# Kernel tuning notes

Hardware: AMD Instinct MI355X
Metric: run time of the kernel (lower is better)

Reference implementation:

```python
import jax, jax.numpy as jnp
import numpy as np
import math

H = 1024
NH = 16
D = H // NH  # 64
EPS = 1e-5


def _layernorm(x, g, b):
    mu = jnp.mean(x, axis=-1, keepdims=True)
    var = jnp.mean(jnp.square(x - mu), axis=-1, keepdims=True)
    return (x - mu) * jax.lax.rsqrt(var + EPS) * g + b


def setup_inputs() -> dict:
    key = jax.random.key(0)
    ks = jax.random.split(key, 12)
    B, T = 2, 2048
    q = jax.random.normal(ks[0], (B, T, H), jnp.float32)
    k = jax.random.normal(ks[1], (B, T, H), jnp.float32)
    v = jax.random.normal(ks[2], (B, T, H), jnp.float32)
    pad_mask = jax.random.randint(ks[3], (B, T), 0, 2) > 0
    s = 0.02
    Wq = jax.random.normal(ks[4], (H, H), jnp.float32) * s
    Wk = jax.random.normal(ks[5], (H, H), jnp.float32) * s
    Wv = jax.random.normal(ks[6], (H, H), jnp.float32) * s
    Wo = jax.random.normal(ks[7], (H, H), jnp.float32) * s
    W1 = jax.random.normal(ks[8], (4 * H, H), jnp.float32) * s
    b1 = jnp.zeros((4 * H,), jnp.float32)
    W2 = jax.random.normal(ks[9], (H, 4 * H), jnp.float32) * s
    b2 = jnp.zeros((H,), jnp.float32)
    g1 = jnp.ones((H,), jnp.float32); be1 = jnp.zeros((H,), jnp.float32)
    g2 = jnp.ones((H,), jnp.float32); be2 = jnp.zeros((H,), jnp.float32)
    return dict(q=q, k=k, v=v, pad_mask=pad_mask, Wq=Wq, Wk=Wk, Wv=Wv, Wo=Wo,
                W1=W1, b1=b1, W2=W2, b2=b2, g1=g1, be1=be1, g2=g2, be2=be2)


def reference(q, k, v, pad_mask, Wq, Wk, Wv, Wo, W1, b1, W2, b2, g1, be1, g2, be2):
    B, Tq, _ = q.shape
    Tv = v.shape[1]
    # torch nn.Linear: x @ W.T
    Q = (q @ Wq.T).reshape(B, NH, Tq, D)  # faithful to torch .view head split
    K = (k @ Wk.T).reshape(B, NH, Tv, D)
    V = (v @ Wv.T).reshape(B, NH, Tv, D)
    logits = jnp.einsum('baih,bajh->baij', Q, K)  # [B,NH,Tq,Tv]
    neg_inf = jnp.float32(-jnp.inf)
    logits = jnp.where(pad_mask[:, None, None, :], logits, neg_inf)
    attn = jax.nn.softmax(logits / math.sqrt(D), axis=-1)
    # post-softmax query-mask multiply (custom)
    attn = attn * pad_mask[:, None, :, None].astype(attn.dtype)
    h = jnp.einsum('baij,bajh->baih', attn, V).reshape(B, Tq, H)
    h = h @ Wo.T
    h = _layernorm(q + h, g1, be1)
    ff = jax.nn.gelu(h @ W1.T + b1, approximate=False) @ W2.T + b2  # dropout = identity (eval)
    return _layernorm(h + ff, g2, be2)
```

## Files before the change

kernel.cpp:

```cpp
#include <hip/hip_runtime.h>

typedef unsigned short u16;
typedef unsigned int u32;
typedef __attribute__((ext_vector_type(8))) __bf16 bf16x8;
typedef __attribute__((ext_vector_type(4))) float f32x4;
typedef __attribute__((ext_vector_type(16))) float f32x16;
typedef __attribute__((ext_vector_type(4))) unsigned short u16x4;
typedef __attribute__((ext_vector_type(8))) unsigned short u16x8;

#define LOG2E 1.44269504088896340736f

__device__ __forceinline__ u16 f2bf(float f) {
  union { float f; unsigned u; } c; c.f = f;
  unsigned r = c.u + 0x7FFFu + ((c.u >> 16) & 1u);
  return (u16)(r >> 16);
}
__device__ __forceinline__ float bf2f(u16 h) {
  union { unsigned u; float f; } c; c.u = ((unsigned)h) << 16;
  return c.f;
}

__device__ __forceinline__ void gload_lds16(const u16* g, u16* l) {
  __builtin_amdgcn_global_load_lds((const __attribute__((address_space(1))) unsigned int*)g,
                                   (__attribute__((address_space(3))) unsigned int*)l, 16, 0, 0);
}

__device__ __forceinline__ float gelu_fast(float x) {
  float z = fabsf(x) * 0.70710678118654752f;
  float t = 1.0f / (1.0f + 0.3275911f * z);
  float poly = t * (0.254829592f + t * (-0.284496736f + t * (1.421413741f +
               t * (-1.453152027f + t * 1.061405429f))));
  float e = __builtin_amdgcn_exp2f(-z * z * LOG2E);
  float erfz = 1.0f - poly * e;
  float s = (x >= 0.0f) ? erfz : -erfz;
  return 0.5f * x * (1.0f + s);
}

__global__ __launch_bounds__(256) void cvt_all(
    const float* __restrict__ s0, const float* __restrict__ s1, const float* __restrict__ s2,
    const float* __restrict__ s3, const float* __restrict__ s4, const float* __restrict__ s5,
    const float* __restrict__ s6, const float* __restrict__ s7, const float* __restrict__ s8,
    u16* __restrict__ d0, u16* __restrict__ d1, u16* __restrict__ d2,
    u16* __restrict__ d3, u16* __restrict__ d4, u16* __restrict__ d5,
    u16* __restrict__ d6, u16* __restrict__ d7, u16* __restrict__ d8) {
  int i = blockIdx.x * 256 + threadIdx.x;
  if (i >= 6291456) return;
  const float* src; u16* dst; int off;
  if (i < 3145728) {
    if (i < 1048576)      { src = s0; dst = d0; off = 0; }
    else if (i < 2097152) { src = s1; dst = d1; off = 1048576; }
    else                  { src = s2; dst = d2; off = 2097152; }
  } else if (i < 4194304) {
    if (i < 3407872)      { src = s3; dst = d3; off = 3145728; }
    else if (i < 3670016) { src = s4; dst = d4; off = 3407872; }
    else if (i < 3932160) { src = s5; dst = d5; off = 3670016; }
    else                  { src = s6; dst = d6; off = 3932160; }
  } else {
    if (i < 5242880)      { src = s7; dst = d7; off = 4194304; }
    else                  { src = s8; dst = d8; off = 5242880; }
  }
  int j = i - off;
  f32x4 v = ((const f32x4*)src)[j];
  u16x4 o;
  o[0] = f2bf(v[0]); o[1] = f2bf(v[1]); o[2] = f2bf(v[2]); o[3] = f2bf(v[3]);
  ((u16x4*)dst)[j] = o;
}

__global__ void build_masks(const void* __restrict__ pm, float* __restrict__ maskbias,
                            float* __restrict__ qmask, int n) {
  __shared__ int sflag;
  if (threadIdx.x == 0) sflag = 0;
  __syncthreads();
  const unsigned* pw = (const unsigned*)pm;
  int nwords = n / 4;
  int local = 0;
  for (int i = threadIdx.x; i < nwords; i += blockDim.x)
    if (pw[i] > 1u) local = 1;
  if (local) atomicOr(&sflag, 1);
  __syncthreads();
  bool isbool = (sflag != 0);
  for (int i = threadIdx.x; i < n; i += blockDim.x) {
    int m = isbool ? (int)((const unsigned char*)pm)[i] : ((const int*)pm)[i];
    maskbias[i] = m ? 0.0f : -2e30f;
    qmask[i]    = m ? 1.0f : 0.0f;
  }
}

template<int EPI>
__device__ __forceinline__ void gemm_core(const u16* __restrict__ A, const u16* __restrict__ Bw,
                                          const float* __restrict__ bias, u16* __restrict__ C,
                                          int N, int Kstride, int Klen, int bn, int bm, int tid) {
  __shared__ u16 smem[3][8192];
  int wave = tid >> 6, lane = tid & 63;
  int l15 = lane & 15, l4 = lane >> 4;
  int wr = (wave >> 1) * 32;
  int wc = (wave & 1) * 64;
  int mrow0 = bm * 128, ncol0 = bn * 128;
  int srow = lane >> 2;
  int scol = (lane & 3) * 8;

  const u16* asrc = A  + (size_t)(mrow0 + wave * 16 + srow) * Kstride + scol;
  const u16* bsrc = Bw + (size_t)(ncol0 + wave * 16 + srow) * Kstride + scol;
  u16* ad = &smem[0][wave * 512];
  u16* bd = &smem[0][4096 + wave * 512];

  auto stage = [&](int buf, int k0) {
    gload_lds16(asrc + k0, ad + buf * 8192);
    gload_lds16(bsrc + k0, bd + buf * 8192);
  };

  f32x4 acc[2][4];
#pragma unroll
  for (int i = 0; i < 2; i++)
#pragma unroll
    for (int j = 0; j < 4; j++) acc[i][j] = (f32x4)0.0f;

  int nsteps = Klen >> 5;
  stage(0, 0);
  stage(1, 32);
  int cur = 0;
  for (int s = 0; s < nsteps; s++) {
    if (s + 1 < nsteps) {
      asm volatile("s_waitcnt vmcnt(2)" ::: "memory");
    } else {
      asm volatile("s_waitcnt vmcnt(0)" ::: "memory");
    }
    __builtin_amdgcn_s_barrier();
    if (s + 2 < nsteps) {
      int nb = cur + 2; if (nb >= 3) nb -= 3;
      stage(nb, (s + 2) << 5);
    }
    const u16* as = &smem[cur][0];
    const u16* bs = &smem[cur][4096];
    bf16x8 af[2], bfr[4];
#pragma unroll
    for (int mi = 0; mi < 2; mi++) af[mi]  = *(const bf16x8*)(as + (wr + mi * 16 + l15) * 32 + l4 * 8);
#pragma unroll
    for (int ni = 0; ni < 4; ni++) bfr[ni] = *(const bf16x8*)(bs + (wc + ni * 16 + l15) * 32 + l4 * 8);
#pragma unroll
    for (int mi = 0; mi < 2; mi++)
#pragma unroll
      for (int ni = 0; ni < 4; ni++)
        acc[mi][ni] = __builtin_amdgcn_mfma_f32_16x16x32_bf16(af[mi], bfr[ni], acc[mi][ni], 0, 0, 0);
    cur++; if (cur >= 3) cur = 0;
  }

  __syncthreads();
  u16* ct = &smem[0][0];
#pragma unroll
  for (int ni = 0; ni < 4; ni++) {
    int gcol = ncol0 + wc + ni * 16 + l15;
    float bv = (EPI > 0) ? bias[gcol] : 0.0f;
#pragma unroll
    for (int mi = 0; mi < 2; mi++) {
#pragma unroll
      for (int r = 0; r < 4; r++) {
        float v = acc[mi][ni][r] + bv;
        if (EPI == 2) v = gelu_fast(v);
        ct[(wr + mi * 16 + l4 * 4 + r) * 136 + wc + ni * 16 + l15] = f2bf(v);
      }
    }
  }
  __syncthreads();
  int lrow = tid >> 2, cq = tid & 3;
#pragma unroll
  for (int j = 0; j < 4; j++) {
    int col = cq * 8 + j * 32;
    u16x8 vv = *(const u16x8*)(ct + lrow * 136 + col);
    *(u16x8*)(C + (size_t)(mrow0 + lrow) * N + ncol0 + col) = vv;
  }
}

template<int EPI>
__global__ __launch_bounds__(512, 4) void gemm_bt(const u16* __restrict__ A, const u16* __restrict__ Bw,
                                                  const float* __restrict__ bias, u16* __restrict__ C,
                                                  int N, int K) {
  gemm_core<EPI>(A, Bw, bias, C, N, K, K, blockIdx.x, blockIdx.y, threadIdx.x);
}

__global__ __launch_bounds__(512, 4) void gemm_splitk(const u16* __restrict__ A, const u16* __restrict__ Bw,
                                                      u16* __restrict__ P, int N, int Kstride, int Kc) {
  int z = blockIdx.z;
  size_t M = (size_t)gridDim.y * 128;
  gemm_core<0>(A + (size_t)z * Kc, Bw + (size_t)z * Kc, nullptr,
               P + (size_t)z * M * N, N, Kstride, Kc, blockIdx.x, blockIdx.y, threadIdx.x);
}

__global__ __launch_bounds__(512, 4) void gemm_qkv(const u16* __restrict__ qb, const u16* __restrict__ kb,
                                                   const u16* __restrict__ vb,
                                                   const u16* __restrict__ wq, const u16* __restrict__ wk,
                                                   const u16* __restrict__ wv,
                                                   u16* __restrict__ Qo, u16* __restrict__ Ko, u16* __restrict__ Vo) {
  const u16* A; const u16* W; u16* C;
  if (blockIdx.z == 0)      { A = qb; W = wq; C = Qo; }
  else if (blockIdx.z == 1) { A = kb; W = wk; C = Ko; }
  else                      { A = vb; W = wv; C = Vo; }
  gemm_core<0>(A, W, nullptr, C, 1024, 1024, 1024, blockIdx.x, blockIdx.y, threadIdx.x);
}

__global__ __launch_bounds__(256) void transpose64(const u16* __restrict__ in, u16* __restrict__ out) {
  int bh = blockIdx.y, tb = blockIdx.x;
  __shared__ u16 tile[64 * 72];
  int tid = threadIdx.x;
#pragma unroll
  for (int it = 0; it < 2; it++) {
    int idx = it * 256 + tid;
    int r = idx >> 3, c8 = (idx & 7) * 8;
    u16x8 v = *(const u16x8*)(in + ((size_t)bh * 2048 + tb * 64 + r) * 64 + c8);
    int byte = ((r * 72 + c8) * 2) ^ (((r >> 3) & 7) << 4);
    *(u16x8*)((char*)tile + byte) = v;
  }
  __syncthreads();
#pragma unroll
  for (int it = 0; it < 2; it++) {
    int idx = it * 256 + tid;
    int d = idx >> 3, t8 = (idx & 7) * 8;
    u16x8 o;
#pragma unroll
    for (int e = 0; e < 8; e++) {
      int t = t8 + e;
      int byte = ((t * 72 + d) * 2) ^ (((t >> 3) & 7) << 4);
      o[e] = *(const u16*)((const char*)tile + byte);
    }
    *(u16x8*)(out + ((size_t)bh * 64 + d) * 2048 + tb * 64 + t8) = o;
  }
}

__global__ __launch_bounds__(256, 4) void attn4(const u16* __restrict__ Q, const u16* __restrict__ Kg,
                                                const u16* __restrict__ VT,
                                                const float* __restrict__ maskbias,
                                                u16* __restrict__ O0, u16* __restrict__ O1,
                                                float* __restrict__ Ms, float* __restrict__ Ss) {
  const int T = 2048;
  int bh = blockIdx.x;
  int qt = blockIdx.y;
  int sp = blockIdx.z;
  int b = bh >> 4;
  const u16* Qh = Q  + (size_t)bh * T * 64;
  const u16* Kh = Kg + (size_t)bh * T * 64;
  const u16* Vh = VT + (size_t)bh * T * 64;
  u16* Oh = (sp ? O1 : O0) + (size_t)bh * T * 64;
  const float* mb = maskbias + b * T + sp * 1024;
  int tid = threadIdx.x, w = tid >> 6, l = tid & 63;
  int q32 = l & 31, h = l >> 5;
  int qbase = qt * 128 + w * 32;
  const float C = 0.125f * LOG2E;

  __shared__ u16 Ks[2][4096];
  __shared__ u16 Vs[2][4096];

  bf16x8 qf[4];
#pragma unroll
  for (int dc = 0; dc < 4; dc++)
    qf[dc] = *(const bf16x8*)(Qh + (size_t)(qbase + q32) * 64 + dc * 16 + h * 8);

  int rl = l >> 3, ob = (l & 7) * 16;
  int osw = ob ^ (rl << 4);
  int r0 = w * 16 + rl, r1 = w * 16 + 8 + rl;
  const u16* pK0 = Kh + (size_t)(sp * 1024 + r0) * 64 + (osw >> 1);
  const u16* pK1 = Kh + (size_t)(sp * 1024 + r1) * 64 + (osw >> 1);
  const u16* pV0 = Vh + (size_t)r0 * 2048 + sp * 1024 + (osw >> 1);
  const u16* pV1 = Vh + (size_t)r1 * 2048 + sp * 1024 + (osw >> 1);
  u16* dK0 = &Ks[0][0] + (w * 16) * 64;
  u16* dK1 = &Ks[0][0] + (w * 16 + 8) * 64;
  u16* dV0 = &Vs[0][0] + (w * 16) * 64;
  u16* dV1 = &Vs[0][0] + (w * 16 + 8) * 64;

  auto stage = [&](int buf) {
    gload_lds16(pK0, dK0 + buf * 4096);
    gload_lds16(pK1, dK1 + buf * 4096);
    gload_lds16(pV0, dV0 + buf * 4096);
    gload_lds16(pV1, dV1 + buf * 4096);
    pK0 += 4096; pK1 += 4096; pV0 += 64; pV1 += 64;
  };

  f32x16 acc[2];
  acc[0] = (f32x16)0.0f; acc[1] = (f32x16)0.0f;
  float m_ = -3e30f, s_ = 0.0f;

  int swz = (q32 & 7) << 4;

  stage(0);
  for (int t = 0; t < 16; t++) {
    int cur = t & 1;
    __syncthreads();
    if (t < 15) stage(cur ^ 1);
    const char* ksb = (const char*)(&Ks[0][0] + cur * 4096);
    const char* vsb = (const char*)(&Vs[0][0] + cur * 4096);

    bf16x8 kf[2][4];
#pragma unroll
    for (int kvc = 0; kvc < 2; kvc++)
#pragma unroll
      for (int dc = 0; dc < 4; dc++)
        kf[kvc][dc] = *(const bf16x8*)(ksb + (kvc * 32 + q32) * 128 + ((dc * 32 + h * 16) ^ swz));

    f32x16 st[2];
    st[0] = (f32x16)0.0f; st[1] = (f32x16)0.0f;
#pragma unroll
    for (int kvc = 0; kvc < 2; kvc++)
#pragma unroll
      for (int dc = 0; dc < 4; dc++)
        st[kvc] = __builtin_amdgcn_mfma_f32_32x32x16_bf16(kf[kvc][dc], qf[dc], st[kvc], 0, 0, 0);

    float p[32];
    float pmax = -3e30f;
#pragma unroll
    for (int kvc = 0; kvc < 2; kvc++) {
#pragma unroll
      for (int g = 0; g < 4; g++) {
        f32x4 mv = *(const f32x4*)(mb + t * 64 + kvc * 32 + g * 8 + h * 4);
#pragma unroll
        for (int r = 0; r < 4; r++) {
          float val = st[kvc][g * 4 + r] * C + mv[r];
          p[kvc * 16 + g * 4 + r] = val;
          pmax = fmaxf(pmax, val);
        }
      }
    }
    pmax = fmaxf(pmax, __shfl_xor(pmax, 32));

    if (__any(pmax - m_ > 8.0f)) {
      float mnew = fmaxf(m_, pmax);
      float fsc = __builtin_amdgcn_exp2f(m_ - mnew);
      s_ *= fsc;
      m_ = mnew;
#pragma unroll
      for (int g = 0; g < 4; g++)
#pragma unroll
        for (int r = 0; r < 4; r++) {
          float f = __shfl(fsc, g * 8 + h * 4 + r);
          acc[0][g * 4 + r] *= f;
          acc[1][g * 4 + r] *= f;
        }
    }

    float rsum = 0.0f;
    u32 wds[16];
#pragma unroll
    for (int i = 0; i < 16; i++) {
      float a = __builtin_amdgcn_exp2f(p[2 * i] - m_);
      float bq = __builtin_amdgcn_exp2f(p[2 * i + 1] - m_);
      rsum += a + bq;
      union { __bf16 h2[2]; u32 u; } cv;
      cv.h2[0] = (__bf16)a; cv.h2[1] = (__bf16)bq;
      wds[i] = cv.u;
    }
    rsum += __shfl_xor(rsum, 32);
    s_ += rsum;

#pragma unroll
    for (int kvc = 0; kvc < 2; kvc++) {
      int bse = kvc * 8;
      u32 sw0 = __shfl_xor(wds[bse + 0], 32), sw1 = __shfl_xor(wds[bse + 1], 32);
      u32 sw2 = __shfl_xor(wds[bse + 2], 32), sw3 = __shfl_xor(wds[bse + 3], 32);
      u32 sw4 = __shfl_xor(wds[bse + 4], 32), sw5 = __shfl_xor(wds[bse + 5], 32);
      u32 sw6 = __shfl_xor(wds[bse + 6], 32), sw7 = __shfl_xor(wds[bse + 7], 32);
      union { u32 u[4]; bf16x8 v; } pa0, pa1;
      pa0.u[0] = h ? sw2 : wds[bse + 0];
      pa0.u[1] = h ? sw3 : wds[bse + 1];
      pa0.u[2] = h ? wds[bse + 2] : sw0;
      pa0.u[3] = h ? wds[bse + 3] : sw1;
      pa1.u[0] = h ? sw6 : wds[bse + 4];
      pa1.u[1] = h ? sw7 : wds[bse + 5];
      pa1.u[2] = h ? wds[bse + 6] : sw4;
      pa1.u[3] = h ? wds[bse + 7] : sw5;
#pragma unroll
      for (int cl = 0; cl < 2; cl++) {
        bf16x8 pa = cl ? pa1.v : pa0.v;
        int cg = kvc * 2 + cl;
#pragma unroll
        for (int dblk = 0; dblk < 2; dblk++) {
          bf16x8 vf = *(const bf16x8*)(vsb + (dblk * 32 + q32) * 128 + ((cg * 32 + h * 16) ^ swz));
          acc[dblk] = __builtin_amdgcn_mfma_f32_32x32x16_bf16(pa, vf, acc[dblk], 0, 0, 0);
        }
      }
    }
  }

#pragma unroll
  for (int g = 0; g < 4; g++) {
#pragma unroll
    for (int r = 0; r < 4; r++) {
      int row = g * 8 + h * 4 + r;
#pragma unroll
      for (int dblk = 0; dblk < 2; dblk++)
        Oh[(size_t)(qbase + row) * 64 + dblk * 32 + q32] = f2bf(acc[dblk][g * 4 + r]);
    }
  }
  if (h == 0) {
    int ro = sp * 65536 + bh * 2048 + qbase + q32;
    Ms[ro] = m_;
    Ss[ro] = s_;
  }
}

__global__ __launch_bounds__(256) void attn_combine(const u16* __restrict__ O0, const u16* __restrict__ O1,
                                                    const float* __restrict__ Ms, const float* __restrict__ Ss,
                                                    const float* __restrict__ qmaskf, u16* __restrict__ out) {
  int idx = blockIdx.x * 256 + threadIdx.x;
  int row = idx >> 3;
  int d8 = (idx & 7) * 8;
  int bh = row >> 11, r = row & 2047, b = bh >> 4;
  float m0 = Ms[row], m1 = Ms[65536 + row];
  float mstar = fmaxf(m0, m1);
  float w0 = __builtin_amdgcn_exp2f(m0 - mstar);
  float w1 = __builtin_amdgcn_exp2f(m1 - mstar);
  float den = w0 * Ss[row] + w1 * Ss[65536 + row];
  float scale = qmaskf[b * 2048 + r] / den;
  size_t base = (size_t)row * 64 + d8;
  u16x8 a0 = *(const u16x8*)(O0 + base);
  u16x8 a1 = *(const u16x8*)(O1 + base);
  u16x8 o;
#pragma unroll
  for (int e = 0; e < 8; e++)
    o[e] = f2bf((w0 * bf2f(a0[e]) + w1 * bf2f(a1[e])) * scale);
  *(u16x8*)(out + base) = o;
}

template<int NP, int A_F32, int ADD_BIAS, int OUT_F32>
__global__ __launch_bounds__(256) void add_ln_multi(const void* __restrict__ Ap,
                                                    const u16* __restrict__ P0, const u16* __restrict__ P1,
                                                    const u16* __restrict__ P2, const u16* __restrict__ P3,
                                                    const float* __restrict__ bias,
                                                    const float* __restrict__ g, const float* __restrict__ be,
                                                    void* __restrict__ outp) {
  int row = blockIdx.x, tid = threadIdx.x;
  int lane = tid & 63, wave = tid >> 6;
  size_t rb = (size_t)row * 1024;
  float x[4];
  if (A_F32) {
    f32x4 a = ((const f32x4*)((const float*)Ap + rb))[tid];
#pragma unroll
    for (int j = 0; j < 4; j++) x[j] = a[j];
  } else {
    u16x4 au = ((const u16x4*)((const u16*)Ap + rb))[tid];
#pragma unroll
    for (int j = 0; j < 4; j++) x[j] = bf2f(au[j]);
  }
  {
    u16x4 p = ((const u16x4*)(P0 + rb))[tid];
#pragma unroll
    for (int j = 0; j < 4; j++) x[j] += bf2f(p[j]);
  }
  if (NP > 1) {
    u16x4 p = ((const u16x4*)(P1 + rb))[tid];
#pragma unroll
    for (int j = 0; j < 4; j++) x[j] += bf2f(p[j]);
  }
  if (NP > 2) {
    u16x4 p = ((const u16x4*)(P2 + rb))[tid];
#pragma unroll
    for (int j = 0; j < 4; j++) x[j] += bf2f(p[j]);
  }
  if (NP > 3) {
    u16x4 p = ((const u16x4*)(P3 + rb))[tid];
#pragma unroll
    for (int j = 0; j < 4; j++) x[j] += bf2f(p[j]);
  }
  if (ADD_BIAS) {
    f32x4 bv = ((const f32x4*)bias)[tid];
#pragma unroll
    for (int j = 0; j < 4; j++) x[j] += bv[j];
  }
  float s = x[0] + x[1] + x[2] + x[3];
  float q = x[0] * x[0] + x[1] * x[1] + x[2] * x[2] + x[3] * x[3];
#pragma unroll
  for (int m = 1; m < 64; m <<= 1) { s += __shfl_xor(s, m); q += __shfl_xor(q, m); }
  __shared__ float rs[4], rq[4];
  if (lane == 0) { rs[wave] = s; rq[wave] = q; }
  __syncthreads();
  float S = rs[0] + rs[1] + rs[2] + rs[3];
  float Qq = rq[0] + rq[1] + rq[2] + rq[3];
  float mean = S * (1.0f / 1024.0f);
  float var = Qq * (1.0f / 1024.0f) - mean * mean;
  float rstd = rsqrtf(var + 1e-5f);
  if (OUT_F32) {
    f32x4 y;
#pragma unroll
    for (int j = 0; j < 4; j++) { int col = tid * 4 + j; y[j] = (x[j] - mean) * rstd * g[col] + be[col]; }
    ((f32x4*)((float*)outp + rb))[tid] = y;
  } else {
    u16x4 y;
#pragma unroll
    for (int j = 0; j < 4; j++) { int col = tid * 4 + j; y[j] = f2bf((x[j] - mean) * rstd * g[col] + be[col]); }
    ((u16x4*)((u16*)outp + rb))[tid] = y;
  }
}

extern "C" void kernel_launch(void* const* d_in, const int* in_sizes, int n_in,
                              void* d_out, int out_size, void* d_ws, size_t ws_size,
                              hipStream_t stream) {
  const float* q   = (const float*)d_in[0];
  const float* k   = (const float*)d_in[1];
  const float* v   = (const float*)d_in[2];
  const void*  pad = d_in[3];
  const float* Wq  = (const float*)d_in[4];
  const float* Wk  = (const float*)d_in[5];
  const float* Wv  = (const float*)d_in[6];
  const float* Wo  = (const float*)d_in[7];
  const float* W1  = (const float*)d_in[8];
  const float* b1  = (const float*)d_in[9];
  const float* W2  = (const float*)d_in[10];
  const float* b2  = (const float*)d_in[11];
  const float* g1  = (const float*)d_in[12];
  const float* be1 = (const float*)d_in[13];
  const float* g2  = (const float*)d_in[14];
  const float* be2 = (const float*)d_in[15];
  float* out = (float*)d_out;
  char* ws = (char*)d_ws;
  const size_t MB = 1u << 20;

  u16* wq_b = (u16*)(ws + 0 * MB);
  u16* wk_b = (u16*)(ws + 2 * MB);
  u16* wv_b = (u16*)(ws + 4 * MB);
  u16* wo_b = (u16*)(ws + 6 * MB);
  u16* w1_b = (u16*)(ws + 8 * MB);
  u16* w2_b = (u16*)(ws + 16 * MB);
  u16* qb   = (u16*)(ws + 24 * MB);
  u16* kb   = (u16*)(ws + 32 * MB);
  u16* vb   = (u16*)(ws + 40 * MB);
  u16* Qb   = (u16*)(ws + 48 * MB);
  u16* Kb   = (u16*)(ws + 56 * MB);
  u16* Vb   = (u16*)(ws + 64 * MB);
  u16* VTb  = (u16*)(ws + 72 * MB);
  u16* hatt = (u16*)(ws + 80 * MB);
  u16* Op0  = (u16*)(ws + 24 * MB);
  u16* Op1  = (u16*)(ws + 32 * MB);
  float* Ms = (float*)(ws + 88 * MB);
  float* Ss = (float*)(ws + 89 * MB);
  u16* WP   = (u16*)(ws + 40 * MB);
  u16* h1b  = (u16*)(ws + 24 * MB);
  u16* ff1  = (u16*)(ws + 32 * MB);
  u16* Fp   = (u16*)(ws + 64 * MB);
  float* maskbias = (float*)(ws + 96 * MB);
  float* qmaskf   = (float*)(ws + 96 * MB + 16384);

  build_masks<<<1, 256, 0, stream>>>(pad, maskbias, qmaskf, in_sizes[3]);

  cvt_all<<<24576, 256, 0, stream>>>(q, k, v, Wq, Wk, Wv, Wo, W1, W2,
                                     qb, kb, vb, wq_b, wk_b, wv_b, wo_b, w1_b, w2_b);

  gemm_qkv<<<dim3(8, 32, 3), 512, 0, stream>>>(qb, kb, vb, wq_b, wk_b, wv_b, Qb, Kb, Vb);

  transpose64<<<dim3(32, 32), 256, 0, stream>>>(Vb, VTb);

  attn4<<<dim3(32, 16, 2), 256, 0, stream>>>(Qb, Kb, VTb, maskbias, Op0, Op1, Ms, Ss);

  attn_combine<<<2048, 256, 0, stream>>>(Op0, Op1, Ms, Ss, qmaskf, hatt);

  gemm_splitk<<<dim3(8, 32, 2), 512, 0, stream>>>(hatt, wo_b, WP, 1024, 1024, 512);

  add_ln_multi<2, 1, 0, 0><<<4096, 256, 0, stream>>>(q, WP, WP + 4194304, nullptr, nullptr,
                                                     nullptr, g1, be1, h1b);

  gemm_bt<2><<<dim3(32, 32), 512, 0, stream>>>(h1b, w1_b, b1, ff1, 4096, 1024);

  gemm_splitk<<<dim3(8, 32, 4), 512, 0, stream>>>(ff1, w2_b, Fp, 1024, 4096, 1024);

  add_ln_multi<4, 0, 1, 1><<<4096, 256, 0, stream>>>(h1b, Fp, Fp + 4194304, Fp + 2 * 4194304,
                                                     Fp + 3 * 4194304, b2, g2, be2, out);
}
```

Measured before the change: 279.1 us.

## Use 64-wide K tiles with swizzled LDS in GEMM and permlane32 swaps in attention

The GEMM core moves from a 3-stage pipeline with 32-wide K steps to a 2-stage double buffer with 64-wide K steps. It uses an XOR-swizzled LDS layout to avoid bank conflicts, which halves the number of barriers per K. In the attention kernel, the 32-lane shuffles for the row max, the row sum and the P-fragment exchange become permlane32_swap instructions. The max reduction also uses a max3 tree. The trade-off is a shallower prefetch depth in the GEMM, with a full vmcnt(0) wait every step, which may expose more load latency.

```diff
diff --git a/kernel.cpp b/kernel.cpp
--- a/kernel.cpp
+++ b/kernel.cpp
@@ -7,6 +7,7 @@
 typedef __attribute__((ext_vector_type(16))) float f32x16;
 typedef __attribute__((ext_vector_type(4))) unsigned short u16x4;
 typedef __attribute__((ext_vector_type(8))) unsigned short u16x8;
+typedef __attribute__((ext_vector_type(2))) int i32x2;
 
 #define LOG2E 1.44269504088896340736f
 
@@ -18,6 +19,9 @@
 __device__ __forceinline__ float bf2f(u16 h) {
   union { unsigned u; float f; } c; c.u = ((unsigned)h) << 16;
   return c.f;
+}
+__device__ __forceinline__ float max3f(float a, float b, float c) {
+  return fmaxf(fmaxf(a, b), c);
 }
 
 __device__ __forceinline__ void gload_lds16(const u16* g, u16* l) {
@@ -90,23 +94,30 @@
 __device__ __forceinline__ void gemm_core(const u16* __restrict__ A, const u16* __restrict__ Bw,
                                           const float* __restrict__ bias, u16* __restrict__ C,
                                           int N, int Kstride, int Klen, int bn, int bm, int tid) {
-  __shared__ u16 smem[3][8192];
+  __shared__ u16 smem[2][16384];
   int wave = tid >> 6, lane = tid & 63;
   int l15 = lane & 15, l4 = lane >> 4;
   int wr = (wave >> 1) * 32;
   int wc = (wave & 1) * 64;
   int mrow0 = bm * 128, ncol0 = bn * 128;
-  int srow = lane >> 2;
-  int scol = (lane & 3) * 8;
-
-  const u16* asrc = A  + (size_t)(mrow0 + wave * 16 + srow) * Kstride + scol;
-  const u16* bsrc = Bw + (size_t)(ncol0 + wave * 16 + srow) * Kstride + scol;
-  u16* ad = &smem[0][wave * 512];
-  u16* bd = &smem[0][4096 + wave * 512];
+  int rl = lane >> 3;
+  int osw = ((lane & 7) * 16) ^ (rl << 4);
+  int oswe = osw >> 1;
+
+  const u16* asrc0 = A  + (size_t)(mrow0 + wave * 16 + rl) * Kstride + oswe;
+  const u16* asrc1 = A  + (size_t)(mrow0 + wave * 16 + 8 + rl) * Kstride + oswe;
+  const u16* bsrc0 = Bw + (size_t)(ncol0 + wave * 16 + rl) * Kstride + oswe;
+  const u16* bsrc1 = Bw + (size_t)(ncol0 + wave * 16 + 8 + rl) * Kstride + oswe;
+  u16* adst0 = &smem[0][wave * 1024];
+  u16* adst1 = &smem[0][wave * 1024 + 512];
+  u16* bdst0 = &smem[0][8192 + wave * 1024];
+  u16* bdst1 = &smem[0][8192 + wave * 1024 + 512];
 
   auto stage = [&](int buf, int k0) {
-    gload_lds16(asrc + k0, ad + buf * 8192);
-    gload_lds16(bsrc + k0, bd + buf * 8192);
+    gload_lds16(asrc0 + k0, adst0 + buf * 16384);
+    gload_lds16(asrc1 + k0, adst1 + buf * 16384);
+    gload_lds16(bsrc0 + k0, bdst0 + buf * 16384);
+    gload_lds16(bsrc1 + k0, bdst1 + buf * 16384);
   };
 
   f32x4 acc[2][4];
@@ -115,34 +126,30 @@
 #pragma unroll
     for (int j = 0; j < 4; j++) acc[i][j] = (f32x4)0.0f;
 
-  int nsteps = Klen >> 5;
+  int nsteps = Klen >> 6;
   stage(0, 0);
-  stage(1, 32);
-  int cur = 0;
+  int swzr = (l15 & 7) << 4;
   for (int s = 0; s < nsteps; s++) {
-    if (s + 1 < nsteps) {
-      asm volatile("s_waitcnt vmcnt(2)" ::: "memory");
-    } else {
-      asm volatile("s_waitcnt vmcnt(0)" ::: "memory");
-    }
+    asm volatile("s_waitcnt vmcnt(0)" ::: "memory");
     __builtin_amdgcn_s_barrier();
-    if (s + 2 < nsteps) {
-      int nb = cur + 2; if (nb >= 3) nb -= 3;
-      stage(nb, (s + 2) << 5);
-    }
-    const u16* as = &smem[cur][0];
-    const u16* bs = &smem[cur][4096];
-    bf16x8 af[2], bfr[4];
-#pragma unroll
-    for (int mi = 0; mi < 2; mi++) af[mi]  = *(const bf16x8*)(as + (wr + mi * 16 + l15) * 32 + l4 * 8);
-#pragma unroll
-    for (int ni = 0; ni < 4; ni++) bfr[ni] = *(const bf16x8*)(bs + (wc + ni * 16 + l15) * 32 + l4 * 8);
-#pragma unroll
-    for (int mi = 0; mi < 2; mi++)
+    if (s + 1 < nsteps) stage((s + 1) & 1, (s + 1) << 6);
+    const char* as = (const char*)&smem[s & 1][0];
+    const char* bs = (const char*)&smem[s & 1][8192];
+#pragma unroll
+    for (int kk = 0; kk < 2; kk++) {
+      bf16x8 af[2], bfr[4];
+#pragma unroll
+      for (int mi = 0; mi < 2; mi++)
+        af[mi]  = *(const bf16x8*)(as + (wr + mi * 16 + l15) * 128 + ((kk * 64 + l4 * 16) ^ swzr));
 #pragma unroll
       for (int ni = 0; ni < 4; ni++)
-        acc[mi][ni] = __builtin_amdgcn_mfma_f32_16x16x32_bf16(af[mi], bfr[ni], acc[mi][ni], 0, 0, 0);
-    cur++; if (cur >= 3) cur = 0;
+        bfr[ni] = *(const bf16x8*)(bs + (wc + ni * 16 + l15) * 128 + ((kk * 64 + l4 * 16) ^ swzr));
+#pragma unroll
+      for (int mi = 0; mi < 2; mi++)
+#pragma unroll
+        for (int ni = 0; ni < 4; ni++)
+          acc[mi][ni] = __builtin_amdgcn_mfma_f32_16x16x32_bf16(af[mi], bfr[ni], acc[mi][ni], 0, 0, 0);
+    }
   }
 
   __syncthreads();
@@ -304,21 +311,26 @@
         st[kvc] = __builtin_amdgcn_mfma_f32_32x32x16_bf16(kf[kvc][dc], qf[dc], st[kvc], 0, 0, 0);
 
     float p[32];
-    float pmax = -3e30f;
 #pragma unroll
     for (int kvc = 0; kvc < 2; kvc++) {
 #pragma unroll
       for (int g = 0; g < 4; g++) {
         f32x4 mv = *(const f32x4*)(mb + t * 64 + kvc * 32 + g * 8 + h * 4);
 #pragma unroll
-        for (int r = 0; r < 4; r++) {
-          float val = st[kvc][g * 4 + r] * C + mv[r];
-          p[kvc * 16 + g * 4 + r] = val;
-          pmax = fmaxf(pmax, val);
-        }
+        for (int r = 0; r < 4; r++)
+          p[kvc * 16 + g * 4 + r] = st[kvc][g * 4 + r] * C + mv[r];
       }
     }
-    pmax = fmaxf(pmax, __shfl_xor(pmax, 32));
+    float ma = p[0], mb2 = p[16];
+#pragma unroll
+    for (int i = 0; i < 7; i++) {
+      ma  = max3f(ma,  p[1 + 2 * i],  p[2 + 2 * i]);
+      mb2 = max3f(mb2, p[17 + 2 * i], p[18 + 2 * i]);
+    }
+    ma = fmaxf(ma, p[15]); mb2 = fmaxf(mb2, p[31]);
+    float pmax = fmaxf(ma, mb2);
+    i32x2 pr = __builtin_amdgcn_permlane32_swap(__float_as_int(pmax), __float_as_int(pmax), false, false);
+    pmax = fmaxf(__int_as_float(pr[0]), __int_as_float(pr[1]));
 
     if (__any(pmax - m_ > 8.0f)) {
       float mnew = fmaxf(m_, pmax);
@@ -346,25 +358,20 @@
       cv.h2[0] = (__bf16)a; cv.h2[1] = (__bf16)bq;
       wds[i] = cv.u;
     }
-    rsum += __shfl_xor(rsum, 32);
+    i32x2 sr = __builtin_amdgcn_permlane32_swap(__float_as_int(rsum), __float_as_int(rsum), false, false);
+    rsum = __int_as_float(sr[0]) + __int_as_float(sr[1]);
     s_ += rsum;
 
 #pragma unroll
     for (int kvc = 0; kvc < 2; kvc++) {
       int bse = kvc * 8;
-      u32 sw0 = __shfl_xor(wds[bse + 0], 32), sw1 = __shfl_xor(wds[bse + 1], 32);
-      u32 sw2 = __shfl_xor(wds[bse + 2], 32), sw3 = __shfl_xor(wds[bse + 3], 32);
-      u32 sw4 = __shfl_xor(wds[bse + 4], 32), sw5 = __shfl_xor(wds[bse + 5], 32);
-      u32 sw6 = __shfl_xor(wds[bse + 6], 32), sw7 = __shfl_xor(wds[bse + 7], 32);
+      i32x2 r02 = __builtin_amdgcn_permlane32_swap((int)wds[bse + 0], (int)wds[bse + 2], false, false);
+      i32x2 r13 = __builtin_amdgcn_permlane32_swap((int)wds[bse + 1], (int)wds[bse + 3], false, false);
+      i32x2 r46 = __builtin_amdgcn_permlane32_swap((int)wds[bse + 4], (int)wds[bse + 6], false, false);
+      i32x2 r57 = __builtin_amdgcn_permlane32_swap((int)wds[bse + 5], (int)wds[bse + 7], false, false);
       union { u32 u[4]; bf16x8 v; } pa0, pa1;
-      pa0.u[0] = h ? sw2 : wds[bse + 0];
-      pa0.u[1] = h ? sw3 : wds[bse + 1];
-      pa0.u[2] = h ? wds[bse + 2] : sw0;
-      pa0.u[3] = h ? wds[bse + 3] : sw1;
-      pa1.u[0] = h ? sw6 : wds[bse + 4];
-      pa1.u[1] = h ? sw7 : wds[bse + 5];
-      pa1.u[2] = h ? wds[bse + 6] : sw4;
-      pa1.u[3] = h ? wds[bse + 7] : sw5;
+      pa0.u[0] = (u32)r02[0]; pa0.u[1] = (u32)r13[0]; pa0.u[2] = (u32)r02[1]; pa0.u[3] = (u32)r13[1];
+      pa1.u[0] = (u32)r46[0]; pa1.u[1] = (u32)r57[0]; pa1.u[2] = (u32)r46[1]; pa1.u[3] = (u32)r57[1];
 #pragma unroll
       for (int cl = 0; cl < 2; cl++) {
         bf16x8 pa = cl ? pa1.v : pa0.v;
```

Result: faster. 271.6 us (median of 2 runs) (-2.7%).
